# Kernel tuning notes

Hardware: AMD Instinct MI355X
Metric: run time of the kernel (lower is better)

Reference implementation:

```python
import jax, jax.numpy as jnp
import numpy as np

N, P, D = 128, 256, 256
H, M = 16, 32            # num_heads, head_dim; output_dim = H*M = 512
OUT, HID = H * M, 2048


def setup_inputs() -> dict:
    key = jax.random.key(0)
    ks = jax.random.split(key, 7)
    s = 0.02
    return {
        "x": jax.random.normal(ks[0], (N, P, D), jnp.float32),
        "qkv_temporal": jax.random.normal(ks[1], (3, D, H, M), jnp.float32) * s,
        "qkv_point": jax.random.normal(ks[2], (3, H, M, H, M), jnp.float32) * s,
        "W1": jax.random.normal(ks[3], (OUT, HID), jnp.float32) * s,
        "b1": jnp.zeros((HID,), jnp.float32),
        "W2": jax.random.normal(ks[4], (HID, OUT), jnp.float32) * s,
        "b2": jnp.zeros((OUT,), jnp.float32),
    }


def reference(x, qkv_temporal, qkv_point, W1, b1, W2, b2):
    # ---- temporal attention (over frames i/I, per point j) ----
    qkv = jnp.einsum('wdhm,ijd->whmij', qkv_temporal, x)     # (3,H,M,N,P)
    q, k, v = qkv[0], qkv[1], qkv[2]
    scores = jnp.einsum('hmij,hmIj->hiIj', q, k)             # (H,N,N,P)
    weights = jax.nn.softmax(scores, axis=2)
    # NOTE: label order 'hIij' (positional) matches the original source exactly
    temporal = jnp.einsum('hIij,hmIj->hmij', weights, v)     # (H,M,N,P)
    # ---- point attention (over points j/J, per frame i) ----
    qkv = jnp.einsum('whmHM,HMij->whmij', qkv_point, temporal)  # (3,H,M,N,P)
    q, k, v = qkv[0], qkv[1], qkv[2]
    scores = jnp.einsum('hmij,hmiJ->hijJ', q, k)             # (H,N,P,P)
    weights = jax.nn.softmax(scores, axis=-1)
    pa = jnp.einsum('hijJ,hmiJ->ijhm', weights, v)           # (N,P,H,M)
    pa = pa.reshape(pa.shape[0], pa.shape[1], -1)            # (N,P,H*M)
    # ---- two-layer MLP (no activation, matching the source) ----
    h = pa @ W1 + b1
    return h @ W2 + b2
```

## Files before the change

kernel.cpp:

```cpp
#include <hip/hip_runtime.h>
#include <cstddef>
#include <cstdint>

constexpr int Nf = 128, Pp = 256, Dd = 256, Hh = 16, Mm = 32;
constexpr int OUTC = 512, HID = 2048, C3 = 1536;

typedef short short8 __attribute__((ext_vector_type(8)));
typedef float f32x4 __attribute__((ext_vector_type(4)));

__device__ inline unsigned short f2bf(float f) {
  unsigned u = __float_as_uint(f);
  u += 0x7fffu + ((u >> 16) & 1u);
  return (unsigned short)(u >> 16);
}
__device__ inline unsigned pk2(float a, float b) {
  return (unsigned)f2bf(a) | ((unsigned)f2bf(b) << 16);
}

__global__ __launch_bounds__(256) void conv_x(const float* __restrict__ x,
                                              short* __restrict__ xb) {
  int idx = blockIdx.x * 256 + threadIdx.x;
  const float4* s = (const float4*)x + (size_t)idx * 2;
  float4 a = s[0], c = s[1];
  uint4 o;
  o.x = pk2(a.x, a.y); o.y = pk2(a.z, a.w);
  o.z = pk2(c.x, c.y); o.w = pk2(c.z, c.w);
  ((uint4*)xb)[idx] = o;
}

__global__ __launch_bounds__(256) void transpose_to_bf16(const float* __restrict__ in,
                                                         short* __restrict__ out,
                                                         int R, int C) {
  __shared__ float tile[64 * 65];
  const int t = threadIdx.x;
  const int rb = blockIdx.y * 64, cb = blockIdx.x * 64;
  const size_t sl = (size_t)blockIdx.z * R * C;
#pragma unroll
  for (int u = 0; u < 4; ++u) {
    int r = (t >> 4) + u * 16, c4 = (t & 15) * 4;
    float4 v = *(const float4*)(in + sl + (size_t)(rb + r) * C + cb + c4);
    tile[r * 65 + c4 + 0] = v.x;
    tile[r * 65 + c4 + 1] = v.y;
    tile[r * 65 + c4 + 2] = v.z;
    tile[r * 65 + c4 + 3] = v.w;
  }
  __syncthreads();
#pragma unroll
  for (int u = 0; u < 2; ++u) {
    int id = t + u * 256;
    int n = id >> 3, kg = id & 7;
    float a[8];
#pragma unroll
    for (int q = 0; q < 8; ++q) a[q] = tile[(kg * 8 + q) * 65 + n];
    uint4 o;
    o.x = pk2(a[0], a[1]); o.y = pk2(a[2], a[3]);
    o.z = pk2(a[4], a[5]); o.w = pk2(a[6], a[7]);
    *(uint4*)(out + sl + (size_t)(cb + n) * R + rb + kg * 8) = o;
  }
}

__global__ void repack_b2t(const float* __restrict__ Wp, short* __restrict__ B2t) {
  int idx = blockIdx.x * 256 + threadIdx.x;
  int c = idx >> 9, k = idx & 511;
  int w = c >> 9, h = (c >> 5) & 15, m = c & 31;
  int HH = k >> 5, MM = k & 31;
  B2t[idx] = (short)f2bf(Wp[(((w * Hh + h) * Mm + m) * Hh + HH) * Mm + MM]);
}

__global__ __launch_bounds__(256) void wc_splitk(const short* __restrict__ A,
                                                 const short* __restrict__ Bt,
                                                 float* __restrict__ part) {
  __shared__ short As[128 * 32];
  __shared__ short Bs[128 * 32];
  const int t = threadIdx.x;
  const int wv = t >> 6, ln = t & 63;
  const int wr = wv >> 1, wc = wv & 1;
  const int lr = ln & 15, kq = ln >> 4;
  const int row0 = blockIdx.y * 128, col0 = blockIdx.x * 128;
  const int k0 = blockIdx.z * 256;

  f32x4 acc[4][4];
#pragma unroll
  for (int i = 0; i < 4; ++i)
#pragma unroll
    for (int j = 0; j < 4; ++j) acc[i][j] = {0.f, 0.f, 0.f, 0.f};

  for (int kt = k0; kt < k0 + 256; kt += 32) {
#pragma unroll
    for (int u = 0; u < 2; ++u) {
      int seg = wv * 128 + u * 64 + ln;
      int r = seg >> 2, kg = seg & 3;
      const short* gp = A + (size_t)(row0 + r) * HID + kt + kg * 8;
      __builtin_amdgcn_global_load_lds(
          (const __attribute__((address_space(1))) void*)gp,
          (__attribute__((address_space(3))) void*)&As[(wv * 128 + u * 64) * 8], 16, 0, 0);
    }
#pragma unroll
    for (int u = 0; u < 2; ++u) {
      int seg = wv * 128 + u * 64 + ln;
      int r = seg >> 2, kg = seg & 3;
      const short* gp = Bt + (size_t)(col0 + r) * HID + kt + kg * 8;
      __builtin_amdgcn_global_load_lds(
          (const __attribute__((address_space(1))) void*)gp,
          (__attribute__((address_space(3))) void*)&Bs[(wv * 128 + u * 64) * 8], 16, 0, 0);
    }
    __syncthreads();
    short8 a[4], b[4];
#pragma unroll
    for (int ti = 0; ti < 4; ++ti)
      a[ti] = *(const short8*)&As[(wr * 64 + ti * 16 + lr) * 32 + kq * 8];
#pragma unroll
    for (int tj = 0; tj < 4; ++tj)
      b[tj] = *(const short8*)&Bs[(wc * 64 + tj * 16 + lr) * 32 + kq * 8];
#pragma unroll
    for (int ti = 0; ti < 4; ++ti)
#pragma unroll
      for (int tj = 0; tj < 4; ++tj)
        acc[ti][tj] = __builtin_amdgcn_mfma_f32_16x16x32_bf16(a[ti], b[tj], acc[ti][tj], 0, 0, 0);
    __syncthreads();
  }

#pragma unroll
  for (int tj = 0; tj < 4; ++tj) {
    int gcol = col0 + wc * 64 + tj * 16 + lr;
#pragma unroll
    for (int ti = 0; ti < 4; ++ti)
#pragma unroll
      for (int rg = 0; rg < 4; ++rg) {
        int grow = row0 + wr * 64 + ti * 16 + kq * 4 + rg;
        part[((size_t)blockIdx.z * 512 + grow) * 512 + gcol] = acc[ti][tj][rg];
      }
  }
}

__global__ __launch_bounds__(256) void wc_reduce(const float* __restrict__ part,
                                                 short* __restrict__ Wct) {
  int idx = blockIdx.x * 256 + threadIdx.x;
  float s = 0.f;
#pragma unroll
  for (int z = 0; z < 8; ++z) s += part[(size_t)z * 262144 + idx];
  Wct[idx] = (short)f2bf(s);
}

__global__ __launch_bounds__(256) void bc_partial(const float* __restrict__ b1,
                                                  const float* __restrict__ W2,
                                                  float* __restrict__ part) {
  const int z = blockIdx.x;
  const int t = threadIdx.x;
  float s0 = 0.f, s1 = 0.f;
#pragma unroll
  for (int hh = 0; hh < 32; ++hh) {
    int h = z * 32 + hh;
    float bv = b1[h];
    s0 += bv * W2[(size_t)h * OUTC + t];
    s1 += bv * W2[(size_t)h * OUTC + t + 256];
  }
  part[z * OUTC + t] = s0;
  part[z * OUTC + t + 256] = s1;
}

__global__ __launch_bounds__(256) void bc_finish(const float* __restrict__ part,
                                                 const float* __restrict__ b2,
                                                 float* __restrict__ bc) {
  int o = blockIdx.x * 256 + threadIdx.x;
  float s = b2[o];
#pragma unroll
  for (int z = 0; z < 64; ++z) s += part[z * OUTC + o];
  bc[o] = s;
}

template <int KDIM, int NCOLS, int AMAP, int EPI, int OUTT>
__global__ __launch_bounds__(256) void gemm_mfma(const short* __restrict__ A,
                                                 const short* __restrict__ Bt,
                                                 void* __restrict__ Cv,
                                                 const float* __restrict__ bias,
                                                 int j0, int pshift, int pc) {
  __shared__ short As[128 * 32];
  __shared__ short Bs[128 * 32];
  const int t = threadIdx.x;
  const int wv = t >> 6, ln = t & 63;
  const int wr = wv >> 1, wc = wv & 1;
  const int lr = ln & 15, kq = ln >> 4;

  constexpr int NBX = NCOLS / 128;
  int lin = blockIdx.y * NBX + blockIdx.x;
  int nblk = gridDim.x * gridDim.y;
  int bx, by;
  if ((nblk & 7) == 0) {
    int per = nblk >> 3;
    int id = (lin & 7) * per + (lin >> 3);
    bx = id % NBX; by = id / NBX;
  } else {
    bx = blockIdx.x; by = blockIdx.y;
  }
  const int row0 = by * 128, col0 = bx * 128;

  f32x4 acc[4][4];
#pragma unroll
  for (int i = 0; i < 4; ++i)
#pragma unroll
    for (int j = 0; j < 4; ++j) acc[i][j] = {0.f, 0.f, 0.f, 0.f};

  for (int kt = 0; kt < KDIM; kt += 32) {
#pragma unroll
    for (int u = 0; u < 2; ++u) {
      int seg = wv * 128 + u * 64 + ln;
      int r = seg >> 2, kg = seg & 3;
      int rr = row0 + r;
      size_t arow;
      if (AMAP == 0) arow = (size_t)rr;
      else { int i = rr >> pshift, jj = rr & (pc - 1); arow = (size_t)((i << 8) + j0 + jj); }
      const short* gp = A + arow * KDIM + kt + kg * 8;
      __builtin_amdgcn_global_load_lds(
          (const __attribute__((address_space(1))) void*)gp,
          (__attribute__((address_space(3))) void*)&As[(wv * 128 + u * 64) * 8], 16, 0, 0);
    }
#pragma unroll
    for (int u = 0; u < 2; ++u) {
      int seg = wv * 128 + u * 64 + ln;
      int r = seg >> 2, kg = seg & 3;
      const short* gp = Bt + (size_t)(col0 + r) * KDIM + kt + kg * 8;
      __builtin_amdgcn_global_load_lds(
          (const __attribute__((address_space(1))) void*)gp,
          (__attribute__((address_space(3))) void*)&Bs[(wv * 128 + u * 64) * 8], 16, 0, 0);
    }
    __syncthreads();
    short8 a[4], b[4];
#pragma unroll
    for (int ti = 0; ti < 4; ++ti)
      a[ti] = *(const short8*)&As[(wr * 64 + ti * 16 + lr) * 32 + kq * 8];
#pragma unroll
    for (int tj = 0; tj < 4; ++tj)
      b[tj] = *(const short8*)&Bs[(wc * 64 + tj * 16 + lr) * 32 + kq * 8];
#pragma unroll
    for (int ti = 0; ti < 4; ++ti)
#pragma unroll
      for (int tj = 0; tj < 4; ++tj)
        acc[ti][tj] = __builtin_amdgcn_mfma_f32_16x16x32_bf16(a[ti], b[tj], acc[ti][tj], 0, 0, 0);
    __syncthreads();
  }

#pragma unroll
  for (int tj = 0; tj < 4; ++tj) {
    int gcol = col0 + wc * 64 + tj * 16 + lr;
    float bv = (EPI == 0) ? bias[gcol] : 0.f;
#pragma unroll
    for (int ti = 0; ti < 4; ++ti) {
#pragma unroll
      for (int rg = 0; rg < 4; ++rg) {
        int grow = row0 + wr * 64 + ti * 16 + kq * 4 + rg;
        float val = acc[ti][tj][rg];
        if (EPI == 0) {
          val += bv;
          if (OUTT == 0) ((short*)Cv)[(size_t)grow * NCOLS + gcol] = (short)f2bf(val);
          else           ((float*)Cv)[(size_t)grow * NCOLS + gcol] = val;
        } else {
          int w = gcol >> 9, h = (gcol >> 5) & 15, m = gcol & 31;
          size_t addr;
          if (EPI == 1) {
            int i = grow >> pshift, jj = grow & (pc - 1);
            addr = (((size_t)(w * Hh + h) * pc + jj) * Nf + i) * Mm + m;
          } else {
            int ii = grow >> 8, j = grow & 255;
            addr = (((size_t)(w * Hh + h) * pc + ii) * Pp + j) * Mm + m;
          }
          ((short*)Cv)[addr] = (short)f2bf(val);
        }
      }
    }
  }
}

__global__ __launch_bounds__(256) void temporal_attn_mfma(const short* __restrict__ T,
                                                          short* __restrict__ At,
                                                          int j0, int jcShift) {
  constexpr int QsO = 0, KsO = 4096, VtO = 8192, WtO = 12544, RsO = 29952;
  __shared__ __align__(16) short lds[30464];
  float* rs = (float*)&lds[RsO];
  const int JC = 1 << jcShift;
  const int h  = blockIdx.x >> jcShift;
  const int jj = blockIdx.x & (JC - 1);
  const int t  = threadIdx.x;
  const int wv = t >> 6, ln = t & 63;
  const int wr = wv >> 1, wc = wv & 1;
  const int lr = ln & 15, kq = ln >> 4;
  const size_t WC = (size_t)(Hh << jcShift) * 4096;
  const short* qb = T + (size_t)(h * JC + jj) * 4096;
  const short* kb = qb + WC;
  const short* vb = qb + 2 * WC;

#pragma unroll
  for (int u = 0; u < 2; ++u) {
    int seg = wv * 2 + u;
    __builtin_amdgcn_global_load_lds(
        (const __attribute__((address_space(1))) void*)(qb + seg * 512 + ln * 8),
        (__attribute__((address_space(3))) void*)&lds[QsO + seg * 512], 16, 0, 0);
    __builtin_amdgcn_global_load_lds(
        (const __attribute__((address_space(1))) void*)(kb + seg * 512 + ln * 8),
        (__attribute__((address_space(3))) void*)&lds[KsO + seg * 512], 16, 0, 0);
  }
#pragma unroll
  for (int u = 0; u < 2; ++u) {
    int idx = t + u * 256;
    int I = idx >> 2, m0 = (idx & 3) * 8;
    uint4 v = *(const uint4*)(vb + idx * 8);
    const short* vs = (const short*)&v;
#pragma unroll
    for (int q = 0; q < 8; ++q) lds[VtO + (m0 + q) * 136 + I] = vs[q];
  }
  __syncthreads();

  short8 af[4], bf[4];
#pragma unroll
  for (int ti = 0; ti < 4; ++ti)
    af[ti] = *(const short8*)&lds[QsO + (wr * 64 + ti * 16 + lr) * 32 + kq * 8];
#pragma unroll
  for (int tj = 0; tj < 4; ++tj)
    bf[tj] = *(const short8*)&lds[KsO + (wc * 64 + tj * 16 + lr) * 32 + kq * 8];
  f32x4 e[4][4];
#pragma unroll
  for (int ti = 0; ti < 4; ++ti)
#pragma unroll
    for (int tj = 0; tj < 4; ++tj) e[ti][tj] = {0.f, 0.f, 0.f, 0.f};
#pragma unroll
  for (int ti = 0; ti < 4; ++ti)
#pragma unroll
    for (int tj = 0; tj < 4; ++tj)
      e[ti][tj] = __builtin_amdgcn_mfma_f32_16x16x32_bf16(af[ti], bf[tj], e[ti][tj], 0, 0, 0);

  float part[4][4];
#pragma unroll
  for (int ti = 0; ti < 4; ++ti)
#pragma unroll
    for (int r = 0; r < 4; ++r) {
      float p = 0.f;
#pragma unroll
      for (int tj = 0; tj < 4; ++tj) {
        float ex = __expf(e[ti][tj][r]);
        e[ti][tj][r] = ex;
        p += ex;
      }
      part[ti][r] = p;
    }
#pragma unroll
  for (int msk = 1; msk <= 8; msk <<= 1)
#pragma unroll
    for (int ti = 0; ti < 4; ++ti)
#pragma unroll
      for (int r = 0; r < 4; ++r)
        part[ti][r] += __shfl_xor(part[ti][r], msk, 64);
  if (lr == 0) {
#pragma unroll
    for (int ti = 0; ti < 4; ++ti)
#pragma unroll
      for (int r = 0; r < 4; ++r)
        rs[wc * 128 + wr * 64 + ti * 16 + kq * 4 + r] = part[ti][r];
  }
  __syncthreads();

#pragma unroll
  for (int ti = 0; ti < 4; ++ti) {
#pragma unroll
    for (int r = 0; r < 4; ++r) {
      int I = wr * 64 + ti * 16 + kq * 4 + r;
      float inv = 1.f / (rs[I] + rs[128 + I]);
#pragma unroll
      for (int tj = 0; tj < 4; ++tj) e[ti][tj][r] *= inv;
    }
#pragma unroll
    for (int tj = 0; tj < 4; ++tj) {
      int i = wc * 64 + tj * 16 + lr;
      int Ib = wr * 64 + ti * 16 + kq * 4;
      uint2 pk;
      pk.x = pk2(e[ti][tj][0], e[ti][tj][1]);
      pk.y = pk2(e[ti][tj][2], e[ti][tj][3]);
      *(uint2*)&lds[WtO + i * 136 + Ib] = pk;
    }
  }
  __syncthreads();

  f32x4 o[2][2];
#pragma unroll
  for (int tr = 0; tr < 2; ++tr)
#pragma unroll
    for (int tm = 0; tm < 2; ++tm) o[tr][tm] = {0.f, 0.f, 0.f, 0.f};
#pragma unroll
  for (int ks = 0; ks < 4; ++ks) {
    short8 ea[2], vf[2];
#pragma unroll
    for (int tr = 0; tr < 2; ++tr)
      ea[tr] = *(const short8*)&lds[WtO + (wv * 32 + tr * 16 + lr) * 136 + ks * 32 + kq * 8];
#pragma unroll
    for (int tm = 0; tm < 2; ++tm)
      vf[tm] = *(const short8*)&lds[VtO + (tm * 16 + lr) * 136 + ks * 32 + kq * 8];
#pragma unroll
    for (int tr = 0; tr < 2; ++tr)
#pragma unroll
      for (int tm = 0; tm < 2; ++tm)
        o[tr][tm] = __builtin_amdgcn_mfma_f32_16x16x32_bf16(ea[tr], vf[tm], o[tr][tm], 0, 0, 0);
  }
#pragma unroll
  for (int tr = 0; tr < 2; ++tr)
#pragma unroll
    for (int tm = 0; tm < 2; ++tm)
#pragma unroll
      for (int r = 0; r < 4; ++r) {
        int row = wv * 32 + tr * 16 + kq * 4 + r;
        lds[row * 40 + tm * 16 + lr] = (short)f2bf(o[tr][tm][r]);
      }
  __syncthreads();
#pragma unroll
  for (int u = 0; u < 2; ++u) {
    int idx = t + u * 256;
    int i = idx >> 2, mg = idx & 3;
    uint4 vv = *(const uint4*)&lds[i * 40 + mg * 8];
    *(uint4*)(At + ((size_t)(i * Pp + j0 + jj) * OUTC + h * 32 + mg * 8)) = vv;
  }
}

__global__ __launch_bounds__(256) void point_attn_mfma(const short* __restrict__ P,
                                                       short* __restrict__ PA,
                                                       int icShift) {
  constexpr int QsO = 0, KsO = 4096, VtO = 8192, EO = 12544, CsO = 29952;
  __shared__ __align__(16) short lds[30720];
  float* cs    = (float*)&lds[CsO];
  float* denom = cs + 256;
  const int IC = 1 << icShift;
  const int bx = blockIdx.x;
  const int h    = bx >> (icShift + 1);
  const int rem  = bx & ((IC << 1) - 1);
  const int ii   = rem >> 1;
  const int half = rem & 1;
  const int t  = threadIdx.x;
  const int wv = t >> 6, ln = t & 63;
  const int wr = wv >> 1, wc = wv & 1;
  const int lr = ln & 15, kq = ln >> 4;
  const size_t WC = (size_t)(Hh << icShift) * 8192;
  const short* qb = P + (size_t)(h * IC + ii) * 8192 + half * 4096;
  const short* kb = P + WC + (size_t)(h * IC + ii) * 8192;
  const short* vb = kb + WC;

  f32x4 o[2][2];
#pragma unroll
  for (int tr = 0; tr < 2; ++tr)
#pragma unroll
    for (int tm = 0; tm < 2; ++tm) o[tr][tm] = {0.f, 0.f, 0.f, 0.f};

  for (int chunk = 0; chunk < 2; ++chunk) {
    const int Jb = chunk * 128;
    if (chunk) __syncthreads();
#pragma unroll
    for (int u = 0; u < 2; ++u) {
      int seg = wv * 2 + u;
      __builtin_amdgcn_global_load_lds(
          (const __attribute__((address_space(1))) void*)(kb + Jb * 32 + seg * 512 + ln * 8),
          (__attribute__((address_space(3))) void*)&lds[KsO + seg * 512], 16, 0, 0);
    }
    if (chunk == 0) {
#pragma unroll
      for (int u = 0; u < 2; ++u) {
        int seg = wv * 2 + u;
        __builtin_amdgcn_global_load_lds(
            (const __attribute__((address_space(1))) void*)(qb + seg * 512 + ln * 8),
            (__attribute__((address_space(3))) void*)&lds[QsO + seg * 512], 16, 0, 0);
      }
      if (t < 128) denom[t] = 0.f;
    }
#pragma unroll
    for (int u = 0; u < 2; ++u) {
      int idx = t + u * 256;
      int Jl = idx >> 2, m0 = (idx & 3) * 8;
      uint4 v = *(const uint4*)(vb + Jb * 32 + idx * 8);
      const short* vs = (const short*)&v;
#pragma unroll
      for (int q = 0; q < 8; ++q) lds[VtO + (m0 + q) * 136 + Jl] = vs[q];
    }
    __syncthreads();

    short8 af[4], bf[4];
#pragma unroll
    for (int ti = 0; ti < 4; ++ti)
      af[ti] = *(const short8*)&lds[KsO + (wr * 64 + ti * 16 + lr) * 32 + kq * 8];
#pragma unroll
    for (int tj = 0; tj < 4; ++tj)
      bf[tj] = *(const short8*)&lds[QsO + (wc * 64 + tj * 16 + lr) * 32 + kq * 8];
    f32x4 e[4][4];
#pragma unroll
    for (int ti = 0; ti < 4; ++ti)
#pragma unroll
      for (int tj = 0; tj < 4; ++tj) e[ti][tj] = {0.f, 0.f, 0.f, 0.f};
#pragma unroll
    for (int ti = 0; ti < 4; ++ti)
#pragma unroll
      for (int tj = 0; tj < 4; ++tj)
        e[ti][tj] = __builtin_amdgcn_mfma_f32_16x16x32_bf16(af[ti], bf[tj], e[ti][tj], 0, 0, 0);

    float cp[4] = {0.f, 0.f, 0.f, 0.f};
#pragma unroll
    for (int ti = 0; ti < 4; ++ti)
#pragma unroll
      for (int tj = 0; tj < 4; ++tj)
#pragma unroll
        for (int r = 0; r < 4; ++r) {
          float ex = __expf(e[ti][tj][r]);
          e[ti][tj][r] = ex;
          cp[tj] += ex;
        }
#pragma unroll
    for (int tj = 0; tj < 4; ++tj) {
      cp[tj] += __shfl_xor(cp[tj], 16, 64);
      cp[tj] += __shfl_xor(cp[tj], 32, 64);
    }
    if (kq == 0) {
#pragma unroll
      for (int tj = 0; tj < 4; ++tj)
        cs[wr * 128 + wc * 64 + tj * 16 + lr] = cp[tj];
    }
#pragma unroll
    for (int ti = 0; ti < 4; ++ti)
#pragma unroll
      for (int tj = 0; tj < 4; ++tj) {
        int j  = wc * 64 + tj * 16 + lr;
        int Jl = wr * 64 + ti * 16 + kq * 4;
        uint2 pk;
        pk.x = pk2(e[ti][tj][0], e[ti][tj][1]);
        pk.y = pk2(e[ti][tj][2], e[ti][tj][3]);
        *(uint2*)&lds[EO + j * 136 + Jl] = pk;
      }
    __syncthreads();
    if (t < 128) denom[t] += cs[t] + cs[128 + t];

#pragma unroll
    for (int ks = 0; ks < 4; ++ks) {
      short8 ea[2], vf[2];
#pragma unroll
      for (int tr = 0; tr < 2; ++tr)
        ea[tr] = *(const short8*)&lds[EO + (wv * 32 + tr * 16 + lr) * 136 + ks * 32 + kq * 8];
#pragma unroll
      for (int tm = 0; tm < 2; ++tm)
        vf[tm] = *(const short8*)&lds[VtO + (tm * 16 + lr) * 136 + ks * 32 + kq * 8];
#pragma unroll
      for (int tr = 0; tr < 2; ++tr)
#pragma unroll
        for (int tm = 0; tm < 2; ++tm)
          o[tr][tm] = __builtin_amdgcn_mfma_f32_16x16x32_bf16(ea[tr], vf[tm], o[tr][tm], 0, 0, 0);
    }
  }
  __syncthreads();

#pragma unroll
  for (int tr = 0; tr < 2; ++tr)
#pragma unroll
    for (int r = 0; r < 4; ++r) {
      int row = wv * 32 + tr * 16 + kq * 4 + r;
      float rinv = 1.f / denom[row];
#pragma unroll
      for (int tm = 0; tm < 2; ++tm)
        lds[row * 40 + tm * 16 + lr] = (short)f2bf(o[tr][tm][r] * rinv);
    }
  __syncthreads();
#pragma unroll
  for (int u = 0; u < 2; ++u) {
    int idx = t + u * 256;
    int jl = idx >> 2, mg = idx & 3;
    uint4 vv = *(const uint4*)&lds[jl * 40 + mg * 8];
    *(uint4*)(PA + ((size_t)(ii * Pp + half * 128 + jl) * OUTC + h * 32 + mg * 8)) = vv;
  }
}

extern "C" void kernel_launch(void* const* d_in, const int* in_sizes, int n_in,
                              void* d_out, int out_size, void* d_ws, size_t ws_size,
                              hipStream_t stream) {
  const float* x  = (const float*)d_in[0];
  const float* Wt = (const float*)d_in[1];
  const float* Wp = (const float*)d_in[2];
  const float* W1 = (const float*)d_in[3];
  const float* b1 = (const float*)d_in[4];
  const float* W2 = (const float*)d_in[5];
  const float* b2 = (const float*)d_in[6];
  float* out = (float*)d_out;
  short* ws  = (short*)d_ws;

  const size_t fixedH = 8388608 + 16777216 + 393216 + 786432 + 1048576 + 1048576
                      + 262144 + 1024 + 4194304 + 65536;
  size_t availH = ws_size / 2;
  size_t chF; int JC, IC;
  if      (availH >= fixedH + 50331648) { chF = 50331648; JC = 256; IC = 128; }
  else if (availH >= fixedH + 12582912) { chF = 12582912; JC = 64;  IC = 32;  }
  else if (availH >= fixedH + 6291456)  { chF = 6291456;  JC = 32;  IC = 16;  }
  else                                  { chF = 3145728;  JC = 16;  IC = 8;   }
  short* CH  = ws;
  short* xbf = CH + chF;
  short* At  = xbf + 8388608;
  short* B1t = At + 16777216;
  short* B2t = B1t + 393216;
  short* W1b = B2t + 786432;
  short* W2t = W1b + 1048576;
  short* Wct = W2t + 1048576;
  float* bcF   = (float*)(Wct + 262144);
  float* partF = (float*)(Wct + 262144 + 1024);
  float* bcP   = (float*)(Wct + 262144 + 1024 + 4194304);
  const int jcS = __builtin_ctz((unsigned)JC);
  const int icS = __builtin_ctz((unsigned)IC);

  conv_x<<<4096, 256, 0, stream>>>(x, xbf);
  conv_x<<<512, 256, 0, stream>>>(W1, W1b);
  transpose_to_bf16<<<dim3(8, 4, 3), 256, 0, stream>>>(Wt, B1t, 256, 512);
  repack_b2t<<<3072, 256, 0, stream>>>(Wp, B2t);
  transpose_to_bf16<<<dim3(8, 32, 1), 256, 0, stream>>>(W2, W2t, 2048, 512);

  wc_splitk<<<dim3(4, 4, 8), 256, 0, stream>>>(W2t, W1b, partF);
  wc_reduce<<<1024, 256, 0, stream>>>(partF, Wct);
  bc_partial<<<64, 256, 0, stream>>>(b1, W2, bcP);
  bc_finish<<<2, 256, 0, stream>>>(bcP, b2, bcF);

  if (JC == 256) {
    gemm_mfma<256, 1536, 0, 1, 0><<<dim3(12, 256), 256, 0, stream>>>(xbf, B1t, CH, nullptr, 0, 8, 256);
    temporal_attn_mfma<<<Hh * 256, 256, 0, stream>>>(CH, At, 0, 8);
    gemm_mfma<512, 1536, 0, 2, 0><<<dim3(12, 256), 256, 0, stream>>>(At, B2t, CH, nullptr, 0, 0, 128);
    point_attn_mfma<<<Hh * 128 * 2, 256, 0, stream>>>(CH, At, 7);
  } else {
    for (int j0 = 0; j0 < Pp; j0 += JC) {
      gemm_mfma<256, 1536, 1, 1, 0><<<dim3(12, JC), 256, 0, stream>>>(xbf, B1t, CH, nullptr, j0, jcS, JC);
      temporal_attn_mfma<<<Hh * JC, 256, 0, stream>>>(CH, At, j0, jcS);
    }
    for (int i0 = 0; i0 < Nf; i0 += IC) {
      short* Arows = At + (size_t)i0 * Pp * OUTC;
      gemm_mfma<512, 1536, 0, 2, 0><<<dim3(12, IC * 2), 256, 0, stream>>>(Arows, B2t, CH, nullptr, 0, 0, IC);
      point_attn_mfma<<<Hh * IC * 2, 256, 0, stream>>>(CH, Arows, icS);
    }
  }

  gemm_mfma<512, 512, 0, 0, 1><<<dim3(4, 256), 256, 0, stream>>>(At, Wct, out, bcF, 0, 0, 0);
}
```

Baseline: 412.1 us.

## Double-buffer LDS tiles in MFMA GEMM with manual waitcnt pipelining

Turns the GEMM main loop into a two-stage pipeline. The next-next K tile is loaded into LDS via global_load_lds while MFMAs run on the current tile, and synchronisation uses explicit vmcnt/lgkmcnt waits and raw s_barrier instead of __syncthreads. Per-thread row addresses are also hoisted out of the loop. This aims to hide global load latency behind the matrix math, at the cost of twice the LDS per block and fragile hand-written waitcnt ordering.

Result: no change. 408.5 us (-0.9%).

```diff
diff --git a/kernel.cpp b/kernel.cpp
--- a/kernel.cpp
+++ b/kernel.cpp
@@ -175,14 +175,15 @@
                                                  void* __restrict__ Cv,
                                                  const float* __restrict__ bias,
                                                  int j0, int pshift, int pc) {
-  __shared__ short As[128 * 32];
-  __shared__ short Bs[128 * 32];
+  __shared__ short As[2][128 * 32];
+  __shared__ short Bs[2][128 * 32];
   const int t = threadIdx.x;
   const int wv = t >> 6, ln = t & 63;
   const int wr = wv >> 1, wc = wv & 1;
   const int lr = ln & 15, kq = ln >> 4;
 
   constexpr int NBX = NCOLS / 128;
+  constexpr int NT = KDIM / 32;
   int lin = blockIdx.y * NBX + blockIdx.x;
   int nblk = gridDim.x * gridDim.y;
   int bx, by;
@@ -195,49 +196,78 @@
   }
   const int row0 = by * 128, col0 = bx * 128;
 
+  const int seg0 = wv * 128 + ln;
+  const int seg1 = wv * 128 + 64 + ln;
+  const int r0 = seg0 >> 2, kg0 = seg0 & 3;
+  const int r1 = seg1 >> 2, kg1 = seg1 & 3;
+  size_t arow0, arow1;
+  {
+    int rr = row0 + r0;
+    if (AMAP == 0) arow0 = (size_t)rr;
+    else { int i = rr >> pshift, jj = rr & (pc - 1); arow0 = (size_t)((i << 8) + j0 + jj); }
+    rr = row0 + r1;
+    if (AMAP == 0) arow1 = (size_t)rr;
+    else { int i = rr >> pshift, jj = rr & (pc - 1); arow1 = (size_t)((i << 8) + j0 + jj); }
+  }
+  const size_t brow0 = (size_t)(col0 + r0), brow1 = (size_t)(col0 + r1);
+
+  auto stage = [&](int buf, int tk) {
+    const int kt = tk * 32;
+    __builtin_amdgcn_global_load_lds(
+        (const __attribute__((address_space(1))) void*)(A + arow0 * KDIM + kt + kg0 * 8),
+        (__attribute__((address_space(3))) void*)&As[buf][(wv * 128) * 8], 16, 0, 0);
+    __builtin_amdgcn_global_load_lds(
+        (const __attribute__((address_space(1))) void*)(A + arow1 * KDIM + kt + kg1 * 8),
+        (__attribute__((address_space(3))) void*)&As[buf][(wv * 128 + 64) * 8], 16, 0, 0);
+    __builtin_amdgcn_global_load_lds(
+        (const __attribute__((address_space(1))) void*)(Bt + brow0 * KDIM + kt + kg0 * 8),
+        (__attribute__((address_space(3))) void*)&Bs[buf][(wv * 128) * 8], 16, 0, 0);
+    __builtin_amdgcn_global_load_lds(
+        (const __attribute__((address_space(1))) void*)(Bt + brow1 * KDIM + kt + kg1 * 8),
+        (__attribute__((address_space(3))) void*)&Bs[buf][(wv * 128 + 64) * 8], 16, 0, 0);
+  };
+
   f32x4 acc[4][4];
 #pragma unroll
   for (int i = 0; i < 4; ++i)
 #pragma unroll
     for (int j = 0; j < 4; ++j) acc[i][j] = {0.f, 0.f, 0.f, 0.f};
 
-  for (int kt = 0; kt < KDIM; kt += 32) {
-#pragma unroll
-    for (int u = 0; u < 2; ++u) {
-      int seg = wv * 128 + u * 64 + ln;
-      int r = seg >> 2, kg = seg & 3;
-      int rr = row0 + r;
-      size_t arow;
-      if (AMAP == 0) arow = (size_t)rr;
-      else { int i = rr >> pshift, jj = rr & (pc - 1); arow = (size_t)((i << 8) + j0 + jj); }
-      const short* gp = A + arow * KDIM + kt + kg * 8;
-      __builtin_amdgcn_global_load_lds(
-          (const __attribute__((address_space(1))) void*)gp,
-          (__attribute__((address_space(3))) void*)&As[(wv * 128 + u * 64) * 8], 16, 0, 0);
-    }
-#pragma unroll
-    for (int u = 0; u < 2; ++u) {
-      int seg = wv * 128 + u * 64 + ln;
-      int r = seg >> 2, kg = seg & 3;
-      const short* gp = Bt + (size_t)(col0 + r) * KDIM + kt + kg * 8;
-      __builtin_amdgcn_global_load_lds(
-          (const __attribute__((address_space(1))) void*)gp,
-          (__attribute__((address_space(3))) void*)&Bs[(wv * 128 + u * 64) * 8], 16, 0, 0);
-    }
-    __syncthreads();
+  stage(0, 0);
+  stage(1, 1);
+  asm volatile("s_waitcnt vmcnt(4)" ::: "memory");
+  __builtin_amdgcn_s_barrier();
+
+  for (int tk = 0; tk < NT; ++tk) {
+    const int cur = tk & 1;
     short8 a[4], b[4];
 #pragma unroll
     for (int ti = 0; ti < 4; ++ti)
-      a[ti] = *(const short8*)&As[(wr * 64 + ti * 16 + lr) * 32 + kq * 8];
+      a[ti] = *(const short8*)&As[cur][(wr * 64 + ti * 16 + lr) * 32 + kq * 8];
 #pragma unroll
     for (int tj = 0; tj < 4; ++tj)
-      b[tj] = *(const short8*)&Bs[(wc * 64 + tj * 16 + lr) * 32 + kq * 8];
+      b[tj] = *(const short8*)&Bs[cur][(wc * 64 + tj * 16 + lr) * 32 + kq * 8];
+    __builtin_amdgcn_sched_barrier(0);
+    asm volatile("s_waitcnt lgkmcnt(0)" ::: "memory");
+    __builtin_amdgcn_sched_barrier(0);
+    if (tk + 1 < NT) {
+      __builtin_amdgcn_s_barrier();
+      if (tk + 2 < NT) stage(cur, tk + 2);
+    }
 #pragma unroll
     for (int ti = 0; ti < 4; ++ti)
 #pragma unroll
       for (int tj = 0; tj < 4; ++tj)
         acc[ti][tj] = __builtin_amdgcn_mfma_f32_16x16x32_bf16(a[ti], b[tj], acc[ti][tj], 0, 0, 0);
-    __syncthreads();
+    if (tk + 1 < NT) {
+      if (tk + 2 < NT) {
+        asm volatile("s_waitcnt vmcnt(4)" ::: "memory");
+      } else {
+        asm volatile("s_waitcnt vmcnt(0)" ::: "memory");
+      }
+      __builtin_amdgcn_s_barrier();
+      __builtin_amdgcn_sched_barrier(0);
+    }
   }
 
 #pragma unroll
```
